# Optimization experiments

Measured on AMD Instinct MI355X. Metric: run time of the kernel, lower is better.

## Reference

```python
import jax, jax.numpy as jnp
import numpy as np

# ---- config (matches init_kwargs) ----
B, C_IN, L, T = 32, 12, 1024, 64
C1, C2, K = 64, 128, 7
PAD = K // 2
NUM_CLASSES = 4
GAIN = 2.0
TH1, TH2 = 0.5, 0.5
TAU1, TAU2 = 1.0, 0.9
RESET = 0.0


def setup_inputs() -> dict:
    key = jax.random.key(0)
    ks = jax.random.split(key, 7)
    x = jax.random.normal(ks[0], (B, C_IN, L, T), dtype=jnp.float32)
    w1 = jax.random.normal(ks[1], (C1, C_IN, K), dtype=jnp.float32) * 0.1
    b1 = jax.random.normal(ks[2], (C1,), dtype=jnp.float32) * 0.01
    w2 = jax.random.normal(ks[3], (C2, C1, K), dtype=jnp.float32) * 0.05
    b2 = jax.random.normal(ks[4], (C2,), dtype=jnp.float32) * 0.01
    fc_w = jax.random.normal(ks[5], (NUM_CLASSES, C2), dtype=jnp.float32) * 0.1
    fc_b = jax.random.normal(ks[6], (NUM_CLASSES,), dtype=jnp.float32) * 0.01
    return {"x": x, "w1": w1, "b1": b1, "w2": w2, "b2": b2, "fc_w": fc_w, "fc_b": fc_b}


def _conv1d(x, w, b):
    # x: [B, Cin, L], w: [Cout, Cin, K] -> [B, Cout, L] (same padding)
    y = jax.lax.conv_general_dilated(
        x, w, window_strides=(1,), padding=[(PAD, PAD)],
        dimension_numbers=("NCW", "OIW", "NCW"))
    return y + b[None, :, None]


def _lif(v, inp, tau, thresh):
    # v <- v + (inp - v)/tau; spike = (v >= thresh); reset spiked neurons
    v = v + (inp - v) / tau
    spike = (v >= thresh).astype(inp.dtype)
    v = jnp.where(spike > 0, jnp.asarray(RESET, inp.dtype), v)
    return v, spike


def reference(x, w1, b1, w2, b2, fc_w, fc_b):
    # QuantStub/DeQuantStub are identity in the fp32 eager model.
    xs = jnp.transpose(x, (3, 0, 1, 2))  # [T, B, C_IN, L]

    def step(carry, xt):
        v1, v2, acc = carry
        h1 = _conv1d(xt, w1, b1) * GAIN
        v1, s1 = _lif(v1, h1, TAU1, TH1)
        h2 = _conv1d(s1, w2, b2) * GAIN
        v2, s2 = _lif(v2, h2, TAU2, TH2)
        return (v1, v2, acc + s2), None

    v1_0 = jnp.zeros((B, C1, L), x.dtype)
    v2_0 = jnp.zeros((B, C2, L), x.dtype)
    acc0 = jnp.zeros((B, C2, L), x.dtype)
    (_, _, acc), _ = jax.lax.scan(step, (v1_0, v2_0, acc0), xs)

    out = acc / jnp.asarray(T, x.dtype)          # [B, C2, L]
    out = jnp.mean(out, axis=-1)                  # AdaptiveAvgPool1d(1) + squeeze
    return out @ fc_w.T + fc_b                    # [B, NUM_CLASSES]
```

## Files before the change

### kernel.cpp

```cpp
#include <hip/hip_runtime.h>
#include <hip/hip_bf16.h>
#include <cstdint>

#define B_   32
#define CIN  12
#define L_   1024
#define T_   64
#define C1_  64
#define C2_  128
#define K_   7
#define PAD_ 3

typedef __attribute__((ext_vector_type(8))) short short8;
typedef __attribute__((ext_vector_type(4))) float float4v;

#define WS_S1T   0ull
#define WS_W2HI  268435456ull
#define WS_W1F   (WS_W2HI + 114688ull)
#define WS_POOL  (WS_W1F + 32768ull)

static __device__ __forceinline__ ushort bf16_hi(float f) {
    __hip_bfloat16 h = __float2bfloat16(f);
    ushort u; __builtin_memcpy(&u, &h, 2); return u;
}
static __device__ __forceinline__ float bf16_back(ushort u) {
    __hip_bfloat16 h; __builtin_memcpy(&h, &u, 2); return __bfloat162float(h);
}

__global__ __launch_bounds__(256) void k0_prep_w2(const float* __restrict__ w2,
                                                  ushort* __restrict__ w2hi,
                                                  float* __restrict__ pool) {
    int i = blockIdx.x * 256 + threadIdx.x;
    if (i < B_ * C2_) pool[i] = 0.0f;
    if (i >= C2_ * K_ * C1_) return;
    int c2 = i / (K_ * C1_);
    int r_ = i % (K_ * C1_);
    int kk = r_ / C1_;
    int c1 = r_ % C1_;
    float w = w2[(c2 * C1_ + c1) * K_ + kk];
    ushort uh = bf16_hi(w);
    int h    = c1 >> 5;
    int c1r  = c1 & 31;
    int e    = c1r >> 4;
    int kq   = (c1r >> 2) & 3;
    int rr   = c1r & 3;
    int j    = e * 4 + rr;
    int mt   = c2 >> 4;
    int lane = kq * 16 + (c2 & 15);
    int o    = ((((kk * 2 + h) * 8 + mt) * 64) + lane) * 8 + j;
    w2hi[o] = uh;
}

__global__ __launch_bounds__(256) void k0_prep_w1(const float* __restrict__ w1,
                                                  ushort* __restrict__ w1f) {
    int i = blockIdx.x * 256 + threadIdx.x;
    if (i >= 16384) return;
    int j    = i & 7;
    int lane = (i >> 3) & 63;
    int mf   = (i >> 9) & 3;
    int ks   = (i >> 11) & 3;
    int cp   = i >> 13;
    int k    = ks * 32 + (lane >> 4) * 8 + j;
    int dl   = k >> 4;
    int slot = k & 15;
    int c1   = mf * 16 + (lane & 15);
    float v  = (slot < CIN && dl < K_) ? w1[(c1 * CIN + slot) * K_ + dl] : 0.0f;
    ushort hi = bf16_hi(v);
    float  rem = v - bf16_back(hi);
    ushort lo = bf16_hi(rem);
    w1f[i] = cp ? lo : hi;
}

__global__ __launch_bounds__(256, 2) void k1_conv1_mfma(const float* __restrict__ x,
                                                        const ushort* __restrict__ w1f,
                                                        const float* __restrict__ b1,
                                                        ushort* __restrict__ s1t) {
    __shared__ __align__(16) ushort S[10 * 2048];
    int tid  = threadIdx.x;
    int lane = tid & 63;
    int wl   = tid >> 6;
    int b    = blockIdx.y;
    int bx   = blockIdx.x;
    int swz  = ((bx & 7) << 5) | (bx >> 3);
    int lb   = swz * 4;

    #pragma unroll
    for (int it = 0; it < 5; ++it) {
        int u  = it * 256 + tid;
        int t  = u & 63;
        int h2 = (u >> 6) & 1;
        int lp = u >> 7;
        int gl = lb + lp - PAD_;
        bool ok = (gl >= 0) && (gl < L_);
        short8 hv, lv;
        #pragma unroll
        for (int jj = 0; jj < 8; ++jj) {
            int cin = h2 * 8 + jj;
            float v = (ok && cin < CIN)
                ? x[(((size_t)b * CIN + cin) * L_ + gl) * T_ + t] : 0.0f;
            ushort hb = bf16_hi(v);
            ushort lo = bf16_hi(v - bf16_back(hb));
            hv[jj] = (short)hb;
            lv[jj] = (short)lo;
        }
        int nt = t >> 4, t15 = t & 15;
        int base = lp * 2048 + nt * 256 + h2 * 128 + t15 * 8;
        *(short8*)&S[base]        = hv;
        *(short8*)&S[base + 1024] = lv;
    }
    __syncthreads();

    int t15 = lane & 15;
    int h2l = (lane >> 4) & 1;
    int kqh = lane >> 5;

    float4v acc[4][4];
    #pragma unroll
    for (int i = 0; i < 4; ++i)
        #pragma unroll
        for (int jn = 0; jn < 4; ++jn)
            acc[i][jn] = (float4v){0.0f, 0.0f, 0.0f, 0.0f};

    #pragma unroll
    for (int ks = 0; ks < 4; ++ks) {
        int dtap = ks * 2 + kqh;
        int lpr  = (dtap == 7) ? 0 : (wl + dtap);
        int rb   = lpr * 2048 + h2l * 128 + t15 * 8;
        short8 bh[4], bl[4];
        #pragma unroll
        for (int nt = 0; nt < 4; ++nt) {
            bh[nt] = *(const short8*)&S[rb + nt * 256];
            bl[nt] = *(const short8*)&S[rb + nt * 256 + 1024];
        }
        #pragma unroll
        for (int mf = 0; mf < 4; ++mf) {
            const ushort* ap = w1f + ((size_t)(ks * 4 + mf) * 64 + lane) * 8;
            short8 ah = *(const short8*)ap;
            short8 al = *(const short8*)(ap + 8192);
            #pragma unroll
            for (int nt = 0; nt < 4; ++nt) {
                acc[mf][nt] = __builtin_amdgcn_mfma_f32_16x16x32_bf16(ah, bh[nt], acc[mf][nt], 0, 0, 0);
                acc[mf][nt] = __builtin_amdgcn_mfma_f32_16x16x32_bf16(al, bh[nt], acc[mf][nt], 0, 0, 0);
                acc[mf][nt] = __builtin_amdgcn_mfma_f32_16x16x32_bf16(ah, bl[nt], acc[mf][nt], 0, 0, 0);
            }
        }
    }

    int l  = lb + wl;
    int kq = lane >> 4;
    #pragma unroll
    for (int h = 0; h < 2; ++h) {
        float4v be0 = *(const float4v*)&b1[h * 32 + kq * 4];
        float4v be1 = *(const float4v*)&b1[h * 32 + 16 + kq * 4];
        #pragma unroll
        for (int nt = 0; nt < 4; ++nt) {
            uint s0 = (acc[2 * h][nt][0] + be0[0] >= 0.25f) ? 0x3F80u : 0u;
            uint s1 = (acc[2 * h][nt][1] + be0[1] >= 0.25f) ? 0x3F80u : 0u;
            uint s2 = (acc[2 * h][nt][2] + be0[2] >= 0.25f) ? 0x3F80u : 0u;
            uint s3 = (acc[2 * h][nt][3] + be0[3] >= 0.25f) ? 0x3F80u : 0u;
            uint s4 = (acc[2 * h + 1][nt][0] + be1[0] >= 0.25f) ? 0x3F80u : 0u;
            uint s5 = (acc[2 * h + 1][nt][1] + be1[1] >= 0.25f) ? 0x3F80u : 0u;
            uint s6 = (acc[2 * h + 1][nt][2] + be1[2] >= 0.25f) ? 0x3F80u : 0u;
            uint s7 = (acc[2 * h + 1][nt][3] + be1[3] >= 0.25f) ? 0x3F80u : 0u;
            uint4 u4 = { s0 | (s1 << 16), s2 | (s3 << 16),
                         s4 | (s5 << 16), s6 | (s7 << 16) };
            size_t off = ((((size_t)b * L_ + l) * 2 + h) * T_ + (nt * 16 + t15)) * 32 + kq * 8;
            *(uint4*)&s1t[off] = u4;
        }
    }
}

__global__ __launch_bounds__(256, 2) void k2_conv2_lif(const ushort* __restrict__ s1t,
                                                       const ushort* __restrict__ w2hi,
                                                       const float* __restrict__ b2,
                                                       float* __restrict__ pool) {
    __shared__ __align__(16) unsigned char lds_raw[32768];
    ushort* S = (ushort*)lds_raw;
    int tid    = threadIdx.x;
    int wv     = tid >> 6;
    int lane   = tid & 63;
    int wm     = wv >> 1;
    int wn     = wv & 1;
    int b      = blockIdx.y;
    int bx     = blockIdx.x;
    int swz    = ((bx & 7) << 6) | (bx >> 3);
    int lb     = swz * 2;
    int lane15 = lane & 15;
    int kq     = lane >> 4;

    float4v acc[4][4];
    #pragma unroll
    for (int i = 0; i < 4; ++i)
        #pragma unroll
        for (int j = 0; j < 4; ++j)
            acc[i][j] = (float4v){0.0f, 0.0f, 0.0f, 0.0f};

    #pragma unroll 1
    for (int h = 0; h < 2; ++h) {
        __syncthreads();
        #pragma unroll
        for (int it = 0; it < 2; ++it) {
            int u  = it * 256 + tid;
            int lp = u >> 6, t = u & 63;
            int gl = lb + lp - PAD_;
            uint4 v0 = {0,0,0,0}, v1 = {0,0,0,0}, v2 = {0,0,0,0}, v3 = {0,0,0,0};
            if (gl >= 0 && gl < L_) {
                const uint4* q = (const uint4*)&s1t[((((size_t)b * L_ + gl) * 2 + h) * T_ + t) * 32];
                v0 = q[0]; v1 = q[1]; v2 = q[2]; v3 = q[3];
            }
            int nt = t >> 4, t15 = t & 15;
            *(uint4*)&S[(((lp * 4 + nt) * 4 + 0) * 16 + t15) * 8] = v0;
            *(uint4*)&S[(((lp * 4 + nt) * 4 + 1) * 16 + t15) * 8] = v1;
            *(uint4*)&S[(((lp * 4 + nt) * 4 + 2) * 16 + t15) * 8] = v2;
            *(uint4*)&S[(((lp * 4 + nt) * 4 + 3) * 16 + t15) * 8] = v3;
        }
        __syncthreads();
        #pragma unroll 2
        for (int kk = 0; kk < K_; ++kk) {
            int lp = wn + kk;
            short8 bf[4];
            #pragma unroll
            for (int nt = 0; nt < 4; ++nt)
                bf[nt] = *(const short8*)&S[(((lp * 4 + nt) * 4) * 16) * 8 + lane * 8];
            #pragma unroll
            for (int mf = 0; mf < 4; ++mf) {
                int aoff = (((kk * 2 + h) * 8 + wm * 4 + mf) * 64 + lane) * 8;
                short8 ahi = *(const short8*)&w2hi[aoff];
                #pragma unroll
                for (int nt = 0; nt < 4; ++nt)
                    acc[mf][nt] = __builtin_amdgcn_mfma_f32_16x16x32_bf16(ahi, bf[nt], acc[mf][nt], 0, 0, 0);
            }
        }
    }
    __syncthreads();

    float* E = ((float*)lds_raw) + wv * 1088;
    int l  = lb + wn;
    int c2 = wm * 64 + lane;
    const float Af = 1.0f - 1.0f / 0.9f;
    const float Cs = 2.0f / 0.9f;
    float D = b2[c2] * Cs;
    float v = 0.0f;
    uint cnt = 0u;
    #pragma unroll
    for (int nt = 0; nt < 4; ++nt) {
        *(float4v*)&E[lane15 * 68 + 0 * 16 + kq * 4] = acc[0][nt];
        *(float4v*)&E[lane15 * 68 + 1 * 16 + kq * 4] = acc[1][nt];
        *(float4v*)&E[lane15 * 68 + 2 * 16 + kq * 4] = acc[2][nt];
        *(float4v*)&E[lane15 * 68 + 3 * 16 + kq * 4] = acc[3][nt];
        __builtin_amdgcn_s_waitcnt(0);
        #pragma unroll
        for (int tt = 0; tt < 16; ++tt) {
            float e = fmaf(E[tt * 68 + lane], Cs, D);
            v = fmaf(Af, v, e);
            bool sp = (v >= 0.5f);
            cnt += sp ? 1u : 0u;
            v = sp ? 0.0f : v;
        }
        __builtin_amdgcn_s_waitcnt(0);
    }
    (void)l;
    atomicAdd(&pool[b * C2_ + c2], (float)cnt);
}

__global__ __launch_bounds__(128) void k3_fc(const float* __restrict__ pool,
                                             const float* __restrict__ fcw,
                                             const float* __restrict__ fcb,
                                             float* __restrict__ out) {
    int i = threadIdx.x;
    int b = i >> 2, c = i & 3;
    float o = fcb[c];
    #pragma unroll 8
    for (int c2 = 0; c2 < C2_; ++c2)
        o = fmaf(fcw[c * C2_ + c2], pool[b * C2_ + c2] * (1.0f / 65536.0f), o);
    out[b * 4 + c] = o;
}

extern "C" void kernel_launch(void* const* d_in, const int* in_sizes, int n_in,
                              void* d_out, int out_size, void* d_ws, size_t ws_size,
                              hipStream_t stream) {
    const float* x   = (const float*)d_in[0];
    const float* w1  = (const float*)d_in[1];
    const float* b1  = (const float*)d_in[2];
    const float* w2  = (const float*)d_in[3];
    const float* b2  = (const float*)d_in[4];
    const float* fcw = (const float*)d_in[5];
    const float* fcb = (const float*)d_in[6];
    float* out = (float*)d_out;

    char* ws = (char*)d_ws;
    ushort* s1t  = (ushort*)(ws + WS_S1T);
    ushort* w2h  = (ushort*)(ws + WS_W2HI);
    ushort* w1f  = (ushort*)(ws + WS_W1F);
    float*  pool = (float*)(ws + WS_POOL);

    k0_prep_w2<<<dim3((C2_ * K_ * C1_ + 255) / 256), dim3(256), 0, stream>>>(w2, w2h, pool);
    k0_prep_w1<<<dim3(64), dim3(256), 0, stream>>>(w1, w1f);
    k1_conv1_mfma<<<dim3(L_ / 4, B_), dim3(256), 0, stream>>>(x, w1f, b1, s1t);
    k2_conv2_lif<<<dim3(L_ / 2, B_), dim3(256), 0, stream>>>(s1t, w2h, b2, pool);
    k3_fc<<<dim3(1), dim3(128), 0, stream>>>(pool, fcw, fcb, out);
}
```

Before: 552.8 us.

## Load conv2 spike B-fragments directly from global, drop LDS staging

The conv2 kernel no longer stages the spike tile into shared memory with block-wide barriers. Each wave now reads its MFMA B fragments straight from global memory, with zeros at the sequence boundaries. LDS use shrinks to the epilogue scratch buffer and launch bounds ask for 4 blocks per CU, aiming for higher occupancy and no sync stalls. The cost is redundant global/L2 reads, since each spike row is reloaded by several waves and taps instead of being shared through LDS.

```diff
diff --git a/kernel.cpp b/kernel.cpp
--- a/kernel.cpp
+++ b/kernel.cpp
@@ -170,12 +170,11 @@
     }
 }
 
-__global__ __launch_bounds__(256, 2) void k2_conv2_lif(const ushort* __restrict__ s1t,
+__global__ __launch_bounds__(256, 4) void k2_conv2_lif(const ushort* __restrict__ s1t,
                                                        const ushort* __restrict__ w2hi,
                                                        const float* __restrict__ b2,
                                                        float* __restrict__ pool) {
-    __shared__ __align__(16) unsigned char lds_raw[32768];
-    ushort* S = (ushort*)lds_raw;
+    __shared__ __align__(16) float E_all[4 * 1088];
     int tid    = threadIdx.x;
     int wv     = tid >> 6;
     int lane   = tid & 63;
@@ -185,8 +184,10 @@
     int bx     = blockIdx.x;
     int swz    = ((bx & 7) << 6) | (bx >> 3);
     int lb     = swz * 2;
+    int l      = lb + wn;
     int lane15 = lane & 15;
     int kq     = lane >> 4;
+    int boff   = lane15 * 32 + kq * 8;
 
     float4v acc[4][4];
     #pragma unroll
@@ -197,31 +198,19 @@
 
     #pragma unroll 1
     for (int h = 0; h < 2; ++h) {
-        __syncthreads();
-        #pragma unroll
-        for (int it = 0; it < 2; ++it) {
-            int u  = it * 256 + tid;
-            int lp = u >> 6, t = u & 63;
-            int gl = lb + lp - PAD_;
-            uint4 v0 = {0,0,0,0}, v1 = {0,0,0,0}, v2 = {0,0,0,0}, v3 = {0,0,0,0};
-            if (gl >= 0 && gl < L_) {
-                const uint4* q = (const uint4*)&s1t[((((size_t)b * L_ + gl) * 2 + h) * T_ + t) * 32];
-                v0 = q[0]; v1 = q[1]; v2 = q[2]; v3 = q[3];
-            }
-            int nt = t >> 4, t15 = t & 15;
-            *(uint4*)&S[(((lp * 4 + nt) * 4 + 0) * 16 + t15) * 8] = v0;
-            *(uint4*)&S[(((lp * 4 + nt) * 4 + 1) * 16 + t15) * 8] = v1;
-            *(uint4*)&S[(((lp * 4 + nt) * 4 + 2) * 16 + t15) * 8] = v2;
-            *(uint4*)&S[(((lp * 4 + nt) * 4 + 3) * 16 + t15) * 8] = v3;
-        }
-        __syncthreads();
         #pragma unroll 2
         for (int kk = 0; kk < K_; ++kk) {
-            int lp = wn + kk;
+            int gl = l + kk - PAD_;
             short8 bf[4];
             #pragma unroll
             for (int nt = 0; nt < 4; ++nt)
-                bf[nt] = *(const short8*)&S[(((lp * 4 + nt) * 4) * 16) * 8 + lane * 8];
+                bf[nt] = (short8){0, 0, 0, 0, 0, 0, 0, 0};
+            if (gl >= 0 && gl < L_) {
+                const ushort* row = &s1t[(((size_t)b * L_ + gl) * 2 + h) * (T_ * 32)];
+                #pragma unroll
+                for (int nt = 0; nt < 4; ++nt)
+                    bf[nt] = *(const short8*)&row[nt * 512 + boff];
+            }
             #pragma unroll
             for (int mf = 0; mf < 4; ++mf) {
                 int aoff = (((kk * 2 + h) * 8 + wm * 4 + mf) * 64 + lane) * 8;
@@ -232,10 +221,8 @@
             }
         }
     }
-    __syncthreads();
-
-    float* E = ((float*)lds_raw) + wv * 1088;
-    int l  = lb + wn;
+
+    float* E = E_all + wv * 1088;
     int c2 = wm * 64 + lane;
     const float Af = 1.0f - 1.0f / 0.9f;
     const float Cs = 2.0f / 0.9f;
@@ -259,7 +246,6 @@
         }
         __builtin_amdgcn_s_waitcnt(0);
     }
-    (void)l;
     atomicAdd(&pool[b * C2_ + c2], (float)cnt);
 }
 
```

After: 702.7 us. 27.1% more time.
